# Optimization experiments

Measured on AMD Instinct MI355X. Metric: run time of the kernel, lower is better.

The kernel has to match this reference:

```python
import jax, jax.numpy as jnp
import numpy as np
import math

HEADS = 32
GROUPS = 8
HEAD_DIM = 64
HIDDEN = 2048
B, S = 2, 2048


def _rope(x, freqs_cis):
    # x: (..., S, head_dim); freqs_cis: (S, head_dim) -> interleaved cos/sin pattern
    x_even = x[..., ::2]
    x_odd = x[..., 1::2]
    cos = freqs_cis[..., ::2]
    sin = freqs_cis[..., 1::2]
    r_even = x_even * cos - x_odd * sin
    r_odd = x_even * sin + x_odd * cos
    return jnp.stack([r_even, r_odd], axis=-1).reshape(x.shape)


def setup_inputs() -> dict:
    key = jax.random.key(0)
    ks = jax.random.split(key, 12)
    scale = 1.0 / math.sqrt(HIDDEN)
    x = jax.random.normal(ks[0], (B, S, HIDDEN), dtype=jnp.float32)
    freqs_cis = jax.random.uniform(ks[1], (S, HEAD_DIM), dtype=jnp.float32)
    causal = jnp.tril(jnp.ones((S, S), dtype=bool))
    mask = jnp.where(causal, 0.0, -1e9).astype(jnp.float32)
    kv_dims = HEAD_DIM * GROUPS
    wq = jax.random.normal(ks[2], (HIDDEN, HIDDEN), jnp.float32) * scale
    bq = jnp.zeros((HIDDEN,), jnp.float32)
    wk = jax.random.normal(ks[3], (kv_dims, HIDDEN), jnp.float32) * scale
    bk = jnp.zeros((kv_dims,), jnp.float32)
    wv = jax.random.normal(ks[4], (kv_dims, HIDDEN), jnp.float32) * scale
    bv = jnp.zeros((kv_dims,), jnp.float32)
    wo = jax.random.normal(ks[5], (HIDDEN, HIDDEN), jnp.float32) * scale
    bo = jnp.zeros((HIDDEN,), jnp.float32)
    return dict(x=x, freqs_cis=freqs_cis, mask=mask, wq=wq, bq=bq,
                wk=wk, bk=bk, wv=wv, bv=bv, wo=wo, bo=bo)


def reference(x, freqs_cis, mask, wq, bq, wk, bk, wv, bv, wo, bo):
    b, s, h = x.shape
    rep = HEADS // GROUPS
    q = x @ wq.T + bq                      # (B,S,H)
    k = x @ wk.T + bk                      # (B,S,G*hd)
    v = x @ wv.T + bv
    q = q.reshape(b, s, HEADS, HEAD_DIM).transpose(0, 2, 1, 3)   # (B,Hh,S,hd)
    k = k.reshape(b, s, GROUPS, HEAD_DIM).transpose(0, 2, 1, 3)  # (B,G,S,hd)
    v = v.reshape(b, s, GROUPS, HEAD_DIM).transpose(0, 2, 1, 3)
    q = _rope(q, freqs_cis)
    k = _rope(k, freqs_cis)
    # GQA: group q heads instead of materially repeating K/V
    qg = q.reshape(b, GROUPS, rep, s, HEAD_DIM)
    scores = jnp.einsum('bgrsd,bgtd->bgrst', qg, k) / math.sqrt(HEAD_DIM)
    scores = scores + mask                 # broadcast (S,S)
    attn = jax.nn.softmax(scores, axis=-1)
    out = jnp.einsum('bgrst,bgtd->bgrsd', attn, v)
    out = out.reshape(b, HEADS, s, HEAD_DIM).transpose(0, 2, 1, 3).reshape(b, s, h)
    return out @ wo.T + bo
```

## Files before the change

### kernel.cpp

```cpp
#include <hip/hip_runtime.h>

#define S_LEN 2048
#define HID   2048
#define NQH   32
#define NKV   8
#define HD    64

#define BM 256
#define BN 128
#define BK 64

typedef __bf16 bf16x8 __attribute__((ext_vector_type(8)));
typedef __bf16 bf16x4 __attribute__((ext_vector_type(4)));
typedef float  f32x4  __attribute__((ext_vector_type(4)));

#define MFMA16(a, b, c) __builtin_amdgcn_mfma_f32_16x16x32_bf16(a, b, c, 0, 0, 0)

__device__ __forceinline__ void async_copy16(const void* g, void* l) {
  __builtin_amdgcn_global_load_lds(
      (const __attribute__((address_space(1))) unsigned int*)g,
      (__attribute__((address_space(3))) unsigned int*)l, 16, 0, 0);
}

__global__ void cast_all_k(const float* __restrict__ x,  const float* __restrict__ wq,
                           const float* __restrict__ wk, const float* __restrict__ wv,
                           const float* __restrict__ wo,
                           __bf16* __restrict__ xb,  __bf16* __restrict__ wqb,
                           __bf16* __restrict__ wkb, __bf16* __restrict__ wvb,
                           __bf16* __restrict__ wob) {
  int bid = blockIdx.x;
  const float* in; __bf16* out; int base;
  if (bid < 8192)       { in = x;  out = xb;  base = bid; }
  else if (bid < 12288) { in = wq; out = wqb; base = bid - 8192; }
  else if (bid < 13312) { in = wk; out = wkb; base = bid - 12288; }
  else if (bid < 14336) { in = wv; out = wvb; base = bid - 13312; }
  else                  { in = wo; out = wob; base = bid - 14336; }
  int i = (base * 256 + threadIdx.x) * 4;
  float4 v = *(const float4*)(in + i);
  bf16x4 o;
  o[0] = (__bf16)v.x; o[1] = (__bf16)v.y; o[2] = (__bf16)v.z; o[3] = (__bf16)v.w;
  *(bf16x4*)(out + i) = o;
}

__device__ __forceinline__ void gemm_pipe(const __bf16* __restrict__ A,
                                          const __bf16* __restrict__ B,
                                          int m0, int n0, int K,
                                          __bf16 (&As)[3][BM][BK],
                                          __bf16 (&Bs)[3][BN][BK],
                                          f32x4 (&acc)[4][4]) {
  const int tid = threadIdx.x, wave = tid >> 6, lane = tid & 63;
  const int l15 = lane & 15, quad = lane >> 4;
  const int wr = wave >> 1, wc = wave & 1;

  const int srow = lane >> 3;
  const int scol = ((lane & 7) ^ srow) * 8;
  const __bf16* ga = A + (size_t)(m0 + wave * 32 + srow) * K + scol;
  const __bf16* gb = B + (size_t)(n0 + wave * 16 + srow) * K + scol;

  const int c0 = ((quad)     ^ (l15 & 7)) * 8;
  const int c1 = ((4 + quad) ^ (l15 & 7)) * 8;

  const int NT = K / BK;

#define STAGE(st, kt) do {                                                        \
    _Pragma("unroll")                                                             \
    for (int i = 0; i < 4; i++)                                                   \
      async_copy16(ga + (kt) + (size_t)(i * 8) * K, &As[st][wave * 32 + i * 8][0]); \
    _Pragma("unroll")                                                             \
    for (int i = 0; i < 2; i++)                                                   \
      async_copy16(gb + (kt) + (size_t)(i * 8) * K, &Bs[st][wave * 16 + i * 8][0]); \
  } while (0)

  STAGE(0, 0);
  STAGE(1, BK);

  int s = 0;
  for (int t = 0; t < NT; t++) {
    if (t + 1 < NT) asm volatile("s_waitcnt vmcnt(6) lgkmcnt(0)" ::: "memory");
    else            asm volatile("s_waitcnt vmcnt(0) lgkmcnt(0)" ::: "memory");
    __builtin_amdgcn_s_barrier();
    asm volatile("" ::: "memory");

    if (t + 2 < NT) {
      int s2 = s + 2; if (s2 >= 3) s2 -= 3;
      STAGE(s2, (t + 2) * BK);
    }

    const __bf16* a0 = &As[s][wr * 64][0];
    const __bf16* b0 = &Bs[s][wc * 64][0];
    bf16x8 af[2][4], bfr[2][4];
#pragma unroll
    for (int mt = 0; mt < 4; mt++) {
      af[0][mt] = *(const bf16x8*)(a0 + (mt * 16 + l15) * BK + c0);
      af[1][mt] = *(const bf16x8*)(a0 + (mt * 16 + l15) * BK + c1);
    }
#pragma unroll
    for (int nt = 0; nt < 4; nt++) {
      bfr[0][nt] = *(const bf16x8*)(b0 + (nt * 16 + l15) * BK + c0);
      bfr[1][nt] = *(const bf16x8*)(b0 + (nt * 16 + l15) * BK + c1);
    }

    __builtin_amdgcn_s_setprio(1);
#pragma unroll
    for (int kk = 0; kk < 2; kk++)
#pragma unroll
      for (int mt = 0; mt < 4; mt++)
#pragma unroll
        for (int nt = 0; nt < 4; nt++)
          acc[mt][nt] = MFMA16(af[kk][mt], bfr[kk][nt], acc[mt][nt]);
    __builtin_amdgcn_s_setprio(0);

    s = s + 1; if (s >= 3) s -= 3;
  }
#undef STAGE
}

__global__ __launch_bounds__(512, 2) void gemm_qkv_k(const __bf16* __restrict__ xb,
    const __bf16* __restrict__ wqb, const __bf16* __restrict__ wkb, const __bf16* __restrict__ wvb,
    const float* __restrict__ bq, const float* __restrict__ bk, const float* __restrict__ bv,
    const float* __restrict__ fr,
    __bf16* __restrict__ Qb, __bf16* __restrict__ Kb, __bf16* __restrict__ Vt) {
  __shared__ __align__(16) __bf16 As[3][BM][BK];
  __shared__ __align__(16) __bf16 Bs[3][BN][BK];
  const int by = blockIdx.y;
  const int m0 = blockIdx.x * BM;
  const __bf16* B; const float* bias; int n0;
  int mode;
  if (by < 16)      { B = wqb; bias = bq; n0 = by * 128;        mode = 0; }
  else if (by < 20) { B = wkb; bias = bk; n0 = (by - 16) * 128; mode = 1; }
  else              { B = wvb; bias = bv; n0 = (by - 20) * 128; mode = 2; }

  f32x4 acc[4][4] = {};
  gemm_pipe(xb, B, m0, n0, HID, As, Bs, acc);

  const int tid = threadIdx.x, wave = tid >> 6, lane = tid & 63;
  const int l15 = lane & 15, quad = lane >> 4;
  const int wr = wave >> 1, wc = wave & 1;

  if (mode == 2) {
#pragma unroll
    for (int nt = 0; nt < 4; nt++) {
      int col = n0 + wc * 64 + nt * 16 + l15;
      int g = col >> 6, d = col & 63;
      float bv2 = bias[col];
#pragma unroll
      for (int mt = 0; mt < 4; mt++) {
        int row = m0 + wr * 64 + mt * 16 + quad * 4;
        int b = row >> 11, sI = row & 2047;
        bf16x4 o;
#pragma unroll
        for (int r = 0; r < 4; r++) o[r] = (__bf16)(acc[mt][nt][r] + bv2);
        *(bf16x4*)(Vt + (((size_t)(b * NKV + g) * HD + d)) * S_LEN + sI) = o;
      }
    }
  } else if (mode == 0) {
#pragma unroll
    for (int nt = 0; nt < 4; nt++) {
      int col = n0 + wc * 64 + nt * 16 + l15;
      float bv2 = bias[col];
#pragma unroll
      for (int mt = 0; mt < 4; mt++) {
        int row = m0 + wr * 64 + mt * 16 + quad * 4;
#pragma unroll
        for (int r = 0; r < 4; r++)
          Qb[(size_t)(row + r) * HID + col] = (__bf16)(acc[mt][nt][r] + bv2);
      }
    }
  } else {
    const int dpar = l15 & 1;
#pragma unroll
    for (int nt = 0; nt < 4; nt++) {
      int col = n0 + wc * 64 + nt * 16 + l15;
      int d = col & 63;
      float bv2 = bias[col];
#pragma unroll
      for (int mt = 0; mt < 4; mt++) {
        int row = m0 + wr * 64 + mt * 16 + quad * 4;
        int sI = row & 2047;
#pragma unroll
        for (int r = 0; r < 4; r++) {
          float v = acc[mt][nt][r] + bv2;
          float p = __shfl_xor(v, 1, 64);
          float f = fr[(size_t)(sI + r) * HD + d];
          float fp = __shfl_xor(f, 1, 64);
          float o = dpar ? (p * f + v * fp) : (v * f - p * fp);
          Kb[(size_t)(row + r) * 512 + col] = (__bf16)o;
        }
      }
    }
  }
}

__global__ __launch_bounds__(512, 2) void gemm_out_k(const __bf16* __restrict__ A,
    const __bf16* __restrict__ Bw, const float* __restrict__ bias, float* __restrict__ C) {
  __shared__ __align__(16) __bf16 As[3][BM][BK];
  __shared__ __align__(16) __bf16 Bs[3][BN][BK];
  const int m0 = blockIdx.x * BM, n0 = blockIdx.y * BN;
  f32x4 acc[4][4] = {};
  gemm_pipe(A, Bw, m0, n0, HID, As, Bs, acc);
  const int tid = threadIdx.x, wave = tid >> 6, lane = tid & 63;
  const int l15 = lane & 15, quad = lane >> 4;
  const int wr = wave >> 1, wc = wave & 1;
#pragma unroll
  for (int nt = 0; nt < 4; nt++) {
    int col = n0 + wc * 64 + nt * 16 + l15;
    float bv = bias[col];
#pragma unroll
    for (int mt = 0; mt < 4; mt++) {
      int row = m0 + wr * 64 + mt * 16 + quad * 4;
#pragma unroll
      for (int r = 0; r < 4; r++)
        C[(size_t)(row + r) * HID + col] = acc[mt][nt][r] + bv;
    }
  }
}

__device__ __forceinline__ void rope8(bf16x8& q, const float* f, float sc) {
  float4 fa = *(const float4*)f;
  float4 fb = *(const float4*)(f + 4);
  float e, o;
  e = (float)q[0]; o = (float)q[1];
  q[0] = (__bf16)((e * fa.x - o * fa.y) * sc);
  q[1] = (__bf16)((e * fa.y + o * fa.x) * sc);
  e = (float)q[2]; o = (float)q[3];
  q[2] = (__bf16)((e * fa.z - o * fa.w) * sc);
  q[3] = (__bf16)((e * fa.w + o * fa.z) * sc);
  e = (float)q[4]; o = (float)q[5];
  q[4] = (__bf16)((e * fb.x - o * fb.y) * sc);
  q[5] = (__bf16)((e * fb.y + o * fb.x) * sc);
  e = (float)q[6]; o = (float)q[7];
  q[6] = (__bf16)((e * fb.z - o * fb.w) * sc);
  q[7] = (__bf16)((e * fb.w + o * fb.z) * sc);
}

__global__ __launch_bounds__(256, 4) void flash_k(const __bf16* __restrict__ Q,
                                                  const __bf16* __restrict__ K,
                                                  const __bf16* __restrict__ Vt,
                                                  const float* __restrict__ fr,
                                                  __bf16* __restrict__ O) {
  __shared__ __align__(64) __bf16 Ksm[64][64];
  __shared__ __align__(64) __bf16 Vsm[64][64];
  __shared__ __align__(64) __bf16 Psm[4][16][64];
  const int tid = threadIdx.x;
  const int wave = tid >> 6, lane = tid & 63;
  const int l15 = lane & 15, quad = lane >> 4;
  const int x7 = l15 & 7, l15h = l15 >> 3;
  const int bh = blockIdx.x;
  const int b = bh >> 5, h = bh & 31, g = h >> 2;

  const int srow = tid >> 2, sc = (tid & 3) * 16;
  const int r7 = srow & 7;
  const int w0 = (((sc >> 3))     ^ r7) * 8;
  const int w1 = (((sc >> 3) + 1) ^ r7) * 8;

  char* kbp = (char*)&Ksm[0][0];
  char* vbp = (char*)&Vsm[0][0];
  char* pbp = (char*)&Psm[0][0][0];
  int kr[2], pr[2], pw[4];
#pragma unroll
  for (int ks = 0; ks < 2; ks++) {
    kr[ks] = l15 * 128 + (((ks * 4 + quad) ^ x7) * 16);
    pr[ks] = wave * 2048 + kr[ks];
  }
#pragma unroll
  for (int nt = 0; nt < 4; nt++)
    pw[nt] = wave * 2048 + quad * 512 + x7 * 2 + (((2 * nt + l15h) ^ ((quad & 1) * 4)) * 16);

  bf16x8 ones;
#pragma unroll
  for (int j = 0; j < 8; j++) ones[j] = (__bf16)1.0f;

  const __bf16* kbase = K + ((size_t)b * S_LEN + srow) * (NKV * HD) + g * HD + sc;
  const __bf16* vbase = Vt + (((size_t)b * NKV + g) * HD + srow) * S_LEN + sc;
  const float QSC = 0.125f * 1.44269504f;

#pragma unroll 1
  for (int half = 0; half < 2; half++) {
    const int qt = half ? (31 - (int)blockIdx.y) : (int)blockIdx.y;
    const int wq0 = qt * 64 + wave * 16;

    const __bf16* qp = Q + ((size_t)(b * S_LEN + wq0 + l15)) * HID + h * HD + quad * 8;
    bf16x8 qf0 = *(const bf16x8*)qp;
    bf16x8 qf1 = *(const bf16x8*)(qp + 32);
    const float* fq = fr + (size_t)(wq0 + l15) * HD + quad * 8;
    rope8(qf0, fq, QSC);
    rope8(qf1, fq + 32, QSC);

    f32x4 acc[4] = {};
    f32x4 accs = {};

    const __bf16* kp = kbase;
    const __bf16* vp = vbase;
    uint4 k0 = *(const uint4*)kp, k1 = *(const uint4*)(kp + 8);
    uint4 v0 = *(const uint4*)vp, v1 = *(const uint4*)(vp + 8);

    for (int t = 0; t <= qt; t++) {
      const int kv0 = t * 64;
      __syncthreads();
      *(uint4*)&Ksm[srow][w0] = k0;
      *(uint4*)&Ksm[srow][w1] = k1;
      *(uint4*)&Vsm[srow][w0] = v0;
      *(uint4*)&Vsm[srow][w1] = v1;
      if (t < qt) {
        kp += 64 * NKV * HD;  vp += 64;
        k0 = *(const uint4*)kp; k1 = *(const uint4*)(kp + 8);
        v0 = *(const uint4*)vp; v1 = *(const uint4*)(vp + 8);
      }
      __syncthreads();

      if (kv0 > wq0 + 15) continue;

      bf16x8 kf[2][4];
#pragma unroll
      for (int ks = 0; ks < 2; ks++)
#pragma unroll
        for (int nt = 0; nt < 4; nt++)
          kf[ks][nt] = *(const bf16x8*)(kbp + (kr[ks] + nt * 2048));

      f32x4 sacc[4] = {};
#pragma unroll
      for (int nt = 0; nt < 4; nt++) {
        sacc[nt] = MFMA16(qf0, kf[0][nt], sacc[nt]);
        sacc[nt] = MFMA16(qf1, kf[1][nt], sacc[nt]);
      }
      const bool domask = (kv0 + 63 > wq0);
#pragma unroll
      for (int nt = 0; nt < 4; nt++) {
        int kv = kv0 + nt * 16 + l15;
        int qr = wq0 + quad * 4;
#pragma unroll
        for (int r = 0; r < 4; r++) {
          float p = __builtin_exp2f(sacc[nt][r]);
          if (domask && kv > qr + r) p = 0.f;
          *(__bf16*)(pbp + ((pw[nt] ^ (r << 4)) + r * 128)) = (__bf16)p;
        }
      }

#pragma unroll
      for (int ks = 0; ks < 2; ks++) {
        bf16x8 vf[4];
#pragma unroll
        for (int nt = 0; nt < 4; nt++)
          vf[nt] = *(const bf16x8*)(vbp + (kr[ks] + nt * 2048));
        bf16x8 pf = *(const bf16x8*)(pbp + pr[ks]);
        accs = MFMA16(pf, ones, accs);
#pragma unroll
        for (int nt = 0; nt < 4; nt++)
          acc[nt] = MFMA16(pf, vf[nt], acc[nt]);
      }
    }

    __bf16* op = O + ((size_t)(b * S_LEN + wq0 + quad * 4)) * HID + h * HD;
    float inv[4];
#pragma unroll
    for (int r = 0; r < 4; r++) inv[r] = 1.f / accs[r];
#pragma unroll
    for (int nt = 0; nt < 4; nt++)
#pragma unroll
      for (int r = 0; r < 4; r++)
        op[(size_t)r * HID + nt * 16 + l15] = (__bf16)(acc[nt][r] * inv[r]);
  }
}

extern "C" void kernel_launch(void* const* d_in, const int* in_sizes, int n_in,
                              void* d_out, int out_size, void* d_ws, size_t ws_size,
                              hipStream_t stream) {
  (void)in_sizes; (void)n_in; (void)out_size; (void)ws_size;
  const float* x  = (const float*)d_in[0];
  const float* fr = (const float*)d_in[1];
  const float* wq = (const float*)d_in[3];
  const float* bq = (const float*)d_in[4];
  const float* wk = (const float*)d_in[5];
  const float* bk = (const float*)d_in[6];
  const float* wv = (const float*)d_in[7];
  const float* bv = (const float*)d_in[8];
  const float* wo = (const float*)d_in[9];
  const float* bo = (const float*)d_in[10];
  float* out = (float*)d_out;
  char* ws = (char*)d_ws;

  __bf16* xb  = (__bf16*)(ws);
  __bf16* wqb = (__bf16*)(ws + ((size_t)16 << 20));
  __bf16* wkb = (__bf16*)(ws + ((size_t)24 << 20));
  __bf16* wvb = (__bf16*)(ws + ((size_t)26 << 20));
  __bf16* wob = (__bf16*)(ws + ((size_t)28 << 20));
  __bf16* Qb  = (__bf16*)(ws + ((size_t)36 << 20));
  __bf16* Kb  = (__bf16*)(ws + ((size_t)52 << 20));
  __bf16* Vtb = (__bf16*)(ws + ((size_t)60 << 20));
  __bf16* Ab  = (__bf16*)(ws + ((size_t)64 << 20));

  cast_all_k<<<18432, 256, 0, stream>>>(x, wq, wk, wv, wo, xb, wqb, wkb, wvb, wob);

  gemm_qkv_k<<<dim3(16, 24), 512, 0, stream>>>(xb, wqb, wkb, wvb, bq, bk, bv, fr, Qb, Kb, Vtb);

  flash_k<<<dim3(64, 16), 256, 0, stream>>>(Qb, Kb, Vtb, fr, Ab);

  gemm_out_k<<<dim3(16, 16), 512, 0, stream>>>(Ab, wob, bo, out);
}
```

Before: 343.5 us.

## Shrink GEMM tiles to 128x128x32 with 4 waves and double buffering

The QKV and output GEMMs move from 256x128x64 tiles with 8 waves and a 3-stage LDS pipeline to 128x128x32 tiles with 4 waves and a 2-stage double buffer. Grids double to 768 and 512 blocks, and launch bounds target 4 blocks per CU. The aim is better CU fill and occupancy, since the old grids (384 and 256 blocks) underfill the GPU. The cost is less data reuse per block, more barriers per K step, and a shallower prefetch that gives less latency hiding.

```diff
diff --git a/kernel.cpp b/kernel.cpp
--- a/kernel.cpp
+++ b/kernel.cpp
@@ -6,9 +6,9 @@
 #define NKV   8
 #define HD    64
 
-#define BM 256
+#define BM 128
 #define BN 128
-#define BK 64
+#define BK 32
 
 typedef __bf16 bf16x8 __attribute__((ext_vector_type(8)));
 typedef __bf16 bf16x4 __attribute__((ext_vector_type(4)));
@@ -45,83 +45,72 @@
 __device__ __forceinline__ void gemm_pipe(const __bf16* __restrict__ A,
                                           const __bf16* __restrict__ B,
                                           int m0, int n0, int K,
-                                          __bf16 (&As)[3][BM][BK],
-                                          __bf16 (&Bs)[3][BN][BK],
+                                          __bf16 (&As)[2][BM][BK],
+                                          __bf16 (&Bs)[2][BN][BK],
                                           f32x4 (&acc)[4][4]) {
   const int tid = threadIdx.x, wave = tid >> 6, lane = tid & 63;
   const int l15 = lane & 15, quad = lane >> 4;
   const int wr = wave >> 1, wc = wave & 1;
 
-  const int srow = lane >> 3;
-  const int scol = ((lane & 7) ^ srow) * 8;
-  const __bf16* ga = A + (size_t)(m0 + wave * 32 + srow) * K + scol;
-  const __bf16* gb = B + (size_t)(n0 + wave * 16 + srow) * K + scol;
-
-  const int c0 = ((quad)     ^ (l15 & 7)) * 8;
-  const int c1 = ((4 + quad) ^ (l15 & 7)) * 8;
+  const int srow   = tid >> 2;
+  const int schunk = (tid & 3) ^ ((tid >> 3) & 3);
+  const __bf16* ga = A + (size_t)(m0 + srow) * K + schunk * 8;
+  const __bf16* gb = B + (size_t)(n0 + srow) * K + schunk * 8;
+
+  const int co = (quad ^ ((l15 >> 1) & 3)) * 8;
 
   const int NT = K / BK;
 
-#define STAGE(st, kt) do {                                                        \
-    _Pragma("unroll")                                                             \
-    for (int i = 0; i < 4; i++)                                                   \
-      async_copy16(ga + (kt) + (size_t)(i * 8) * K, &As[st][wave * 32 + i * 8][0]); \
-    _Pragma("unroll")                                                             \
-    for (int i = 0; i < 2; i++)                                                   \
-      async_copy16(gb + (kt) + (size_t)(i * 8) * K, &Bs[st][wave * 16 + i * 8][0]); \
+#define STAGE(st, kt) do {                                              \
+    async_copy16(ga + (kt),                  &As[st][wave * 16][0]);    \
+    async_copy16(ga + (kt) + (size_t)64 * K, &As[st][64 + wave * 16][0]); \
+    async_copy16(gb + (kt),                  &Bs[st][wave * 16][0]);    \
+    async_copy16(gb + (kt) + (size_t)64 * K, &Bs[st][64 + wave * 16][0]); \
   } while (0)
 
   STAGE(0, 0);
-  STAGE(1, BK);
+  asm volatile("s_waitcnt vmcnt(0)" ::: "memory");
+  __builtin_amdgcn_s_barrier();
+  asm volatile("" ::: "memory");
 
   int s = 0;
+#pragma unroll 2
   for (int t = 0; t < NT; t++) {
-    if (t + 1 < NT) asm volatile("s_waitcnt vmcnt(6) lgkmcnt(0)" ::: "memory");
-    else            asm volatile("s_waitcnt vmcnt(0) lgkmcnt(0)" ::: "memory");
+    if (t + 1 < NT) STAGE(s ^ 1, (t + 1) * BK);
+
+    const __bf16* a0 = &As[s][wr * 64][0];
+    const __bf16* b0 = &Bs[s][wc * 64][0];
+    bf16x8 af[4], bfr[4];
+#pragma unroll
+    for (int mt = 0; mt < 4; mt++)
+      af[mt] = *(const bf16x8*)(a0 + (mt * 16 + l15) * BK + co);
+#pragma unroll
+    for (int nt = 0; nt < 4; nt++)
+      bfr[nt] = *(const bf16x8*)(b0 + (nt * 16 + l15) * BK + co);
+
+    __builtin_amdgcn_s_setprio(1);
+#pragma unroll
+    for (int mt = 0; mt < 4; mt++)
+#pragma unroll
+      for (int nt = 0; nt < 4; nt++)
+        acc[mt][nt] = MFMA16(af[mt], bfr[nt], acc[mt][nt]);
+    __builtin_amdgcn_s_setprio(0);
+
+    asm volatile("s_waitcnt vmcnt(0) lgkmcnt(0)" ::: "memory");
     __builtin_amdgcn_s_barrier();
     asm volatile("" ::: "memory");
-
-    if (t + 2 < NT) {
-      int s2 = s + 2; if (s2 >= 3) s2 -= 3;
-      STAGE(s2, (t + 2) * BK);
-    }
-
-    const __bf16* a0 = &As[s][wr * 64][0];
-    const __bf16* b0 = &Bs[s][wc * 64][0];
-    bf16x8 af[2][4], bfr[2][4];
-#pragma unroll
-    for (int mt = 0; mt < 4; mt++) {
-      af[0][mt] = *(const bf16x8*)(a0 + (mt * 16 + l15) * BK + c0);
-      af[1][mt] = *(const bf16x8*)(a0 + (mt * 16 + l15) * BK + c1);
-    }
-#pragma unroll
-    for (int nt = 0; nt < 4; nt++) {
-      bfr[0][nt] = *(const bf16x8*)(b0 + (nt * 16 + l15) * BK + c0);
-      bfr[1][nt] = *(const bf16x8*)(b0 + (nt * 16 + l15) * BK + c1);
-    }
-
-    __builtin_amdgcn_s_setprio(1);
-#pragma unroll
-    for (int kk = 0; kk < 2; kk++)
-#pragma unroll
-      for (int mt = 0; mt < 4; mt++)
-#pragma unroll
-        for (int nt = 0; nt < 4; nt++)
-          acc[mt][nt] = MFMA16(af[kk][mt], bfr[kk][nt], acc[mt][nt]);
-    __builtin_amdgcn_s_setprio(0);
-
-    s = s + 1; if (s >= 3) s -= 3;
+    s ^= 1;
   }
 #undef STAGE
 }
 
-__global__ __launch_bounds__(512, 2) void gemm_qkv_k(const __bf16* __restrict__ xb,
+__global__ __launch_bounds__(256, 4) void gemm_qkv_k(const __bf16* __restrict__ xb,
     const __bf16* __restrict__ wqb, const __bf16* __restrict__ wkb, const __bf16* __restrict__ wvb,
     const float* __restrict__ bq, const float* __restrict__ bk, const float* __restrict__ bv,
     const float* __restrict__ fr,
     __bf16* __restrict__ Qb, __bf16* __restrict__ Kb, __bf16* __restrict__ Vt) {
-  __shared__ __align__(16) __bf16 As[3][BM][BK];
-  __shared__ __align__(16) __bf16 Bs[3][BN][BK];
+  __shared__ __align__(16) __bf16 As[2][BM][BK];
+  __shared__ __align__(16) __bf16 Bs[2][BN][BK];
   const int by = blockIdx.y;
   const int m0 = blockIdx.x * BM;
   const __bf16* B; const float* bias; int n0;
@@ -191,10 +180,10 @@
   }
 }
 
-__global__ __launch_bounds__(512, 2) void gemm_out_k(const __bf16* __restrict__ A,
+__global__ __launch_bounds__(256, 4) void gemm_out_k(const __bf16* __restrict__ A,
     const __bf16* __restrict__ Bw, const float* __restrict__ bias, float* __restrict__ C) {
-  __shared__ __align__(16) __bf16 As[3][BM][BK];
-  __shared__ __align__(16) __bf16 Bs[3][BN][BK];
+  __shared__ __align__(16) __bf16 As[2][BM][BK];
+  __shared__ __align__(16) __bf16 Bs[2][BN][BK];
   const int m0 = blockIdx.x * BM, n0 = blockIdx.y * BN;
   f32x4 acc[4][4] = {};
   gemm_pipe(A, Bw, m0, n0, HID, As, Bs, acc);
@@ -391,9 +380,9 @@
 
   cast_all_k<<<18432, 256, 0, stream>>>(x, wq, wk, wv, wo, xb, wqb, wkb, wvb, wob);
 
-  gemm_qkv_k<<<dim3(16, 24), 512, 0, stream>>>(xb, wqb, wkb, wvb, bq, bk, bv, fr, Qb, Kb, Vtb);
+  gemm_qkv_k<<<dim3(32, 24), 256, 0, stream>>>(xb, wqb, wkb, wvb, bq, bk, bv, fr, Qb, Kb, Vtb);
 
   flash_k<<<dim3(64, 16), 256, 0, stream>>>(Qb, Kb, Vtb, fr, Ab);
 
-  gemm_out_k<<<dim3(16, 16), 512, 0, stream>>>(Ab, wob, bo, out);
-}
+  gemm_out_k<<<dim3(32, 16), 256, 0, stream>>>(Ab, wob, bo, out);
+}
```

Result: faster. 315.2 us (-8.2%).
